# Kernel tuning notes

Hardware: AMD Instinct MI355X
Metric: run time of the kernel (lower is better)

## Reference

```python
import math
import jax, jax.numpy as jnp
import numpy as np

NUM_HEADS, RAD_PTS, LVL_PTS = 8, 4, 1
P = RAD_PTS * LVL_PTS


def setup_inputs() -> dict:
    B, Nq, Din = 2, 21760, 256
    hw = np.array([[128, 128], [64, 64], [32, 32], [16, 16]], np.int64)
    sizes = hw[:, 0] * hw[:, 1]
    offs = np.concatenate([[0], np.cumsum(sizes)[:-1]]).astype(np.int64)
    Ns = int(sizes.sum())
    map_ids = np.tile(np.repeat(np.arange(4), sizes)[None], (B, 1)).astype(np.int64)

    key = jax.random.key(0)
    ks = jax.random.split(key, 8)
    in_feats = jax.random.normal(ks[0], (B, Nq, Din), jnp.float32)
    sample_feats = jax.random.normal(ks[1], (B, Ns, Din), jnp.float32)
    sample_priors = jax.random.uniform(ks[2], (B, Nq, 2), jnp.float32)

    # sample_offsets bias: radial grid init as in the torch module
    thetas = np.arange(NUM_HEADS) * (2.0 * math.pi / NUM_HEADS)
    grid = np.stack([np.cos(thetas), np.sin(thetas), np.zeros(NUM_HEADS)], 1)
    grid = grid / np.abs(grid).max(1, keepdims=True)
    grid = np.tile(grid.reshape(NUM_HEADS, 1, 1, 3), (1, RAD_PTS, LVL_PTS, 1))
    grid = grid * np.arange(1, RAD_PTS + 1).reshape(1, RAD_PTS, 1, 1)
    bo = jnp.asarray(grid.reshape(-1), jnp.float32)

    Wo = jax.random.normal(ks[3], (NUM_HEADS * P * 3, Din), jnp.float32) * 0.01
    Wa = jax.random.normal(ks[4], (NUM_HEADS * P, Din), jnp.float32) * 0.01
    ba = jnp.zeros((NUM_HEADS * P,), jnp.float32)
    s = 1.0 / np.sqrt(Din)
    Wv = jax.random.normal(ks[5], (Din, Din), jnp.float32) * s
    bv = jnp.zeros((Din,), jnp.float32)
    Wout = jax.random.normal(ks[6], (Din, Din), jnp.float32) * s
    bout = jnp.zeros((Din,), jnp.float32)

    return dict(in_feats=in_feats, sample_priors=sample_priors, sample_feats=sample_feats,
                map_hw=jnp.asarray(hw), map_offs=jnp.asarray(offs), map_ids=jnp.asarray(map_ids),
                Wo=Wo, bo=bo, Wa=Wa, ba=ba, Wv=Wv, bv=bv, Wout=Wout, bout=bout)


def _trilinear_sample(val, map_hw, map_offs, xy, z, L):
    # val [B,Ns,H,D]; xy [B,Q,H,P,2] normalized; z [B,Q,H,P] in ~[0,1]
    B, Ns, H, D = val.shape
    Q = xy.shape[1]
    val_t = val.transpose(0, 2, 1, 3)  # [B,H,Ns,D]
    x, y = xy[..., 0], xy[..., 1]
    lvl_f = z * (L - 1)
    l0 = jnp.floor(lvl_f).astype(jnp.int32)
    wz = lvl_f - l0.astype(lvl_f.dtype)

    def gather(idx):  # idx [B,Q,H,P] int32 -> [B,Q,H,P,D]
        it = idx.transpose(0, 2, 1, 3).reshape(B, H, Q * P, 1)
        g = jnp.take_along_axis(val_t, it, axis=2)  # [B,H,Q*P,D]
        return g.reshape(B, H, Q, P, D).transpose(0, 2, 1, 3, 4)

    def sample_level(lvl):  # bilinear sample within pyramid level `lvl` (zero padding)
        valid_l = (lvl >= 0) & (lvl < L)
        lc = jnp.clip(lvl, 0, L - 1)
        Hl = map_hw[lc, 0].astype(jnp.int32)
        Wl = map_hw[lc, 1].astype(jnp.int32)
        off = map_offs[lc].astype(jnp.int32)
        xf = x * Wl.astype(x.dtype) - 0.5
        yf = y * Hl.astype(x.dtype) - 0.5
        x0 = jnp.floor(xf).astype(jnp.int32)
        y0 = jnp.floor(yf).astype(jnp.int32)
        dx = xf - x0.astype(x.dtype)
        dy = yf - y0.astype(x.dtype)
        out = jnp.zeros((B, Q, H, P, D), x.dtype)
        corners = [(x0, y0, (1 - dx) * (1 - dy)), (x0 + 1, y0, dx * (1 - dy)),
                   (x0, y0 + 1, (1 - dx) * dy), (x0 + 1, y0 + 1, dx * dy)]
        for xi, yi, w in corners:
            ok = valid_l & (xi >= 0) & (xi < Wl) & (yi >= 0) & (yi < Hl)
            idx = off + jnp.clip(yi, 0, Hl - 1) * Wl + jnp.clip(xi, 0, Wl - 1)
            out = out + gather(idx) * (w * ok.astype(x.dtype))[..., None]
        return out

    return sample_level(l0) * (1 - wz)[..., None] + sample_level(l0 + 1) * wz[..., None]


def reference(in_feats, sample_priors, sample_feats, map_hw, map_offs, map_ids,
              Wo, bo, Wa, ba, Wv, bv, Wout, bout):
    B, Nq, _ = in_feats.shape
    Ns = sample_feats.shape[1]
    L = map_hw.shape[0]
    D = Wv.shape[0] // NUM_HEADS

    val = (sample_feats @ Wv.T + bv).reshape(B, Ns, NUM_HEADS, D)
    offs = (in_feats @ Wo.T + bo).reshape(B, Nq, NUM_HEADS, P, 3)

    # sample_priors last dim == 2: normalize offsets by (W, H) of the query's map
    norm = map_hw[:, ::-1][map_ids].astype(offs.dtype)  # [B,Nq,2] (w,h)
    sample_xy = sample_priors[:, :, None, None, :2] + offs[..., :2] / norm[:, :, None, None, :]

    lvl_off = jnp.arange(LVL_PTS, dtype=offs.dtype) - 0.5 * (LVL_PTS - 1)
    z_grid = map_ids[:, :, None, None, None].astype(offs.dtype) + lvl_off  # [B,Nq,1,1,Lp]
    z_grid = jnp.broadcast_to(z_grid, (B, Nq, NUM_HEADS, RAD_PTS, LVL_PTS)).reshape(B, Nq, NUM_HEADS, P)
    sample_z = (z_grid + jnp.tanh(offs[..., 2])) / (L - 1)

    attn = jax.nn.softmax((in_feats @ Wa.T + ba).reshape(B, Nq, NUM_HEADS, P), axis=3)

    sampled = _trilinear_sample(val, map_hw, map_offs, sample_xy, sample_z, L)  # [B,Nq,H,P,D]
    attn_feats = jnp.einsum('bqhpd,bqhp->bqhd', sampled, attn).reshape(B, Nq, NUM_HEADS * D)
    return attn_feats @ Wout.T + bout
```

## Files before the change

kernel.cpp:

```cpp
#include <hip/hip_runtime.h>
#include <hip/hip_bf16.h>
#include <math.h>

typedef __bf16 bf16x8 __attribute__((ext_vector_type(8)));
typedef float f32x4 __attribute__((ext_vector_type(4)));
typedef float f32x2 __attribute__((ext_vector_type(2)));
typedef unsigned short ushort8 __attribute__((ext_vector_type(8)));

static __device__ __forceinline__ unsigned short f2bf(float f) {
    union { float f; unsigned u; } c; c.f = f;
    unsigned r = c.u + 0x7FFFu + ((c.u >> 16) & 1u);
    return (unsigned short)(r >> 16);
}

static __device__ __forceinline__ void gload_lds16(
    const unsigned short* g, unsigned short* l)
{
    __builtin_amdgcn_global_load_lds(
        (const __attribute__((address_space(1))) void*)g,
        (__attribute__((address_space(3))) void*)l, 16, 0, 0);
}

__global__ __launch_bounds__(256) void convert_weights_hist(
    const float* __restrict__ Wv, const float* __restrict__ Wo,
    const float* __restrict__ Wa, const float* __restrict__ Wout,
    const float* __restrict__ bo, const float* __restrict__ ba,
    unsigned short* __restrict__ Wv_b, unsigned short* __restrict__ Woa_b,
    unsigned short* __restrict__ Wout_b, float* __restrict__ boa,
    const float* __restrict__ priors, int* __restrict__ counts,
    int BQ, int Nq)
{
    __shared__ int cnt[16];
    if (threadIdx.x < 16) cnt[threadIdx.x] = 0;
    __syncthreads();

    int gid = blockIdx.x * blockDim.x + threadIdx.x;
    int stride = gridDim.x * blockDim.x;
    for (int i = gid; i < 163840; i += stride) {
        if (i < 65536)       Wv_b[i] = f2bf(Wv[i]);
        else if (i < 90112)  Woa_b[i - 65536] = f2bf(Wo[i - 65536]);
        else if (i < 98304)  Woa_b[i - 65536] = f2bf(Wa[i - 90112]);
        else                 Wout_b[i - 98304] = f2bf(Wout[i - 98304]);
    }
    if (gid < 96)       boa[gid] = bo[gid];
    else if (gid < 128) boa[gid] = ba[gid - 96];

    for (int q = gid; q < BQ; q += stride) {
        int b = (q >= Nq) ? 1 : 0;
        float py = priors[(size_t)q * 2 + 1];
        int band = min(7, max(0, (int)(py * 8.0f)));
        atomicAdd(&cnt[b * 8 + band], 1);
    }
    __syncthreads();
    if (threadIdx.x < 16 && cnt[threadIdx.x] > 0)
        atomicAdd(&counts[threadIdx.x], cnt[threadIdx.x]);
}

__global__ __launch_bounds__(256) void bucket_scatter(
    const float* __restrict__ priors, const int* __restrict__ counts,
    int* __restrict__ cursors, int* __restrict__ qidx, int BQ, int Nq)
{
    __shared__ int lcnt[16];
    __shared__ int lbase[16];
    const int tid = threadIdx.x;
    if (tid < 16) lcnt[tid] = 0;
    __syncthreads();
    int q = blockIdx.x * 256 + tid;
    int mybucket = 0, myslot = 0;
    bool valid = q < BQ;
    if (valid) {
        int b = (q >= Nq) ? 1 : 0;
        float py = priors[(size_t)q * 2 + 1];
        int band = min(7, max(0, (int)(py * 8.0f)));
        mybucket = b * 8 + band;
        myslot = atomicAdd(&lcnt[mybucket], 1);
    }
    __syncthreads();
    if (tid < 16) {
        int base = 0;
        #pragma unroll
        for (int i = 0; i < 16; ++i) base += (i < tid) ? counts[i] : 0;
        lbase[tid] = base + atomicAdd(&cursors[tid], lcnt[tid]);
    }
    __syncthreads();
    if (valid) qidx[lbase[mybucket] + myslot] = q;
}

template<int WM, int WN, bool A_BF16, int OUT_MODE>
__global__ __launch_bounds__(WM * WN * 64) void gemm_mfma(
    const void* __restrict__ Av, const unsigned short* __restrict__ W,
    const float* __restrict__ bias, void* __restrict__ Cv,
    int M, int N, int K, int NsPB)
{
    constexpr int BM = WM * 64;
    constexpr int BN = WN * 64;
    constexpr int BK = 64;
    constexpr int NWAVE = WM * WN;
    constexpr int NTHR = NWAVE * 64;
    constexpr int LDP = 72;
    constexpr int ASZ = A_BF16 ? (BM * 64) : (BM * LDP);

    __shared__ __align__(16) unsigned short As[ASZ];
    __shared__ __align__(16) unsigned short Bs[BN * 64];

    const int bm  = blockIdx.x * BM;
    const int bn  = blockIdx.y * BN;
    const int tid = threadIdx.x;
    const int wid = tid >> 6;
    const int wrow = wid / WN;
    const int wcol = wid % WN;
    const int lane = tid & 63;
    const int lr = lane & 15;
    const int lg = lane >> 4;
    const int lrow = lane >> 3;
    const int lc16 = (lane & 7) ^ (lrow & 7);

    f32x4 acc[4][4];
    #pragma unroll
    for (int mi = 0; mi < 4; ++mi)
        #pragma unroll
        for (int ni = 0; ni < 4; ++ni)
            acc[mi][ni] = (f32x4){0.f, 0.f, 0.f, 0.f};

    for (int kt = 0; kt < K; kt += BK) {
        #pragma unroll
        for (int c = wid; c < BN / 8; c += NWAVE) {
            const unsigned short* g =
                W + (size_t)(bn + c * 8 + lrow) * K + kt + lc16 * 8;
            gload_lds16(g, Bs + c * 512);
        }
        if (A_BF16) {
            const unsigned short* A = (const unsigned short*)Av;
            #pragma unroll
            for (int c = wid; c < BM / 8; c += NWAVE) {
                const unsigned short* g =
                    A + (size_t)(bm + c * 8 + lrow) * K + kt + lc16 * 8;
                gload_lds16(g, As + c * 512);
            }
        } else {
            const float* A = (const float*)Av;
            #pragma unroll
            for (int u = tid; u < BM * 8; u += NTHR) {
                int r = u >> 3, kb = u & 7;
                const float* src = A + (size_t)(bm + r) * K + kt + kb * 8;
                float4 f0 = *(const float4*)(src);
                float4 f1 = *(const float4*)(src + 4);
                ushort8 v;
                v[0] = f2bf(f0.x); v[1] = f2bf(f0.y);
                v[2] = f2bf(f0.z); v[3] = f2bf(f0.w);
                v[4] = f2bf(f1.x); v[5] = f2bf(f1.y);
                v[6] = f2bf(f1.z); v[7] = f2bf(f1.w);
                *(ushort8*)(As + r * LDP + kb * 8) = v;
            }
        }
        __syncthreads();

        #pragma unroll
        for (int kk = 0; kk < 2; ++kk) {
            bf16x8 fa[4], fb[4];
            #pragma unroll
            for (int mi = 0; mi < 4; ++mi) {
                int row = wrow * 64 + mi * 16 + lr;
                if (A_BF16) {
                    fa[mi] = *(const bf16x8*)(As + row * 64 +
                                              ((kk * 4 + lg) ^ (lr & 7)) * 8);
                } else {
                    fa[mi] = *(const bf16x8*)(As + row * LDP +
                                              kk * 32 + lg * 8);
                }
            }
            #pragma unroll
            for (int ni = 0; ni < 4; ++ni) {
                int row = wcol * 64 + ni * 16 + lr;
                fb[ni] = *(const bf16x8*)(Bs + row * 64 +
                                          ((kk * 4 + lg) ^ (lr & 7)) * 8);
            }
            #pragma unroll
            for (int mi = 0; mi < 4; ++mi)
                #pragma unroll
                for (int ni = 0; ni < 4; ++ni)
                    acc[mi][ni] = __builtin_amdgcn_mfma_f32_16x16x32_bf16(
                        fa[mi], fb[ni], acc[mi][ni], 0, 0, 0);
        }
        __syncthreads();
    }

    if (OUT_MODE == 2) {
        const int b = bm / NsPB;
        const int ns_base = bm - b * NsPB;
        #pragma unroll
        for (int ni = 0; ni < 4; ++ni) {
            int col = wcol * 64 + ni * 16 + lr;
            int h   = col >> 5;
            int ch  = col & 31;
            float bv = bias[col];
            unsigned short* dst = (unsigned short*)Cv +
                (size_t)(b * 8 + h) * NsPB * 32 + ch;
            #pragma unroll
            for (int mi = 0; mi < 4; ++mi) {
                #pragma unroll
                for (int r = 0; r < 4; ++r) {
                    int ns = ns_base + mi * 16 + lg * 4 + r;
                    dst[(size_t)ns * 32] = f2bf(acc[mi][ni][r] + bv);
                }
            }
        }
    } else {
        #pragma unroll
        for (int ni = 0; ni < 4; ++ni) {
            int col = bn + wcol * 64 + ni * 16 + lr;
            float bv = bias[col];
            #pragma unroll
            for (int mi = 0; mi < 4; ++mi) {
                #pragma unroll
                for (int r = 0; r < 4; ++r) {
                    int row = bm + wrow * 64 + mi * 16 + lg * 4 + r;
                    if (OUT_MODE == 1) {
                        ((unsigned short*)Cv)[(size_t)row * N + col] =
                            f2bf(acc[mi][ni][r] + bv);
                    } else {
                        ((float*)Cv)[(size_t)row * N + col] = acc[mi][ni][r] + bv;
                    }
                }
            }
        }
    }
}

__global__ __launch_bounds__(256) void msda_sample_kernel(
    const float* __restrict__ C1,
    const float* __restrict__ priors,
    const unsigned short* __restrict__ val,
    const int*   __restrict__ map_hw,
    const int*   __restrict__ map_offs,
    const int*   __restrict__ map_ids,
    const int*   __restrict__ qidx,
    unsigned short* __restrict__ out,
    int Nq, int Ns)
{
    const int swz  = (blockIdx.x & 7) * (gridDim.x >> 3) + (blockIdx.x >> 3);
    const int wvi  = threadIdx.x >> 6;
    const int lane = threadIdx.x & 63;
    const int qbase = swz * 16 + wvi * 4;

    __shared__ __align__(16) float s_rec[4][4][4][128];

    const int hp = lane >> 1;
    const int sl = lane & 1;

    int bq4[4];
    #pragma unroll
    for (int qq = 0; qq < 4; ++qq) bq4[qq] = qidx[qbase + qq];

    float o0[4], o1[4], o2[4], lgt[4], px[4], py[4];
    int bb[4], lid[4];
    #pragma unroll
    for (int qq = 0; qq < 4; ++qq) {
        const int bq = bq4[qq];
        const int b  = (bq >= Nq) ? 1 : 0;
        const int q  = bq - b * Nq;
        bb[qq] = b;
        const float* sc = C1 + (size_t)bq * 128;
        o0[qq]  = sc[hp * 3 + 0];
        o1[qq]  = sc[hp * 3 + 1];
        o2[qq]  = sc[hp * 3 + 2];
        lgt[qq] = sc[96 + hp];
        px[qq]  = priors[(size_t)bq * 2 + 0];
        py[qq]  = priors[(size_t)bq * 2 + 1];
        lid[qq] = map_ids[(size_t)b * Ns + q];
    }

    #pragma unroll
    for (int qq = 0; qq < 4; ++qq) {
        float logit = lgt[qq];
        float m = logit;
        m = fmaxf(m, __shfl_xor(m, 2));
        m = fmaxf(m, __shfl_xor(m, 4));
        float e = expf(logit - m);
        float s = e;
        s += __shfl_xor(s, 2);
        s += __shfl_xor(s, 4);
        float attnw = e / s;

        int Hq = map_hw[lid[qq] * 2 + 0];
        int Wq = map_hw[lid[qq] * 2 + 1];
        float x = px[qq] + o0[qq] / (float)Wq;
        float y = py[qq] + o1[qq] / (float)Hq;

        float lvl_f = (float)lid[qq] + tanhf(o2[qq]);
        float l0f = floorf(lvl_f);
        int   l0  = (int)l0f;
        float wz  = lvl_f - l0f;

        const int   lv = l0 + sl;
        const float wl = sl ? wz : (1.0f - wz);
        float w4[4];
        int   i4[4];
        if (lv >= 0 && lv < 4) {
            int Hs  = map_hw[lv * 2 + 0];
            int Ws  = map_hw[lv * 2 + 1];
            int off = map_offs[lv];
            float xf = x * (float)Ws - 0.5f;
            float yf = y * (float)Hs - 0.5f;
            float x0f = floorf(xf), y0f = floorf(yf);
            int   x0  = (int)x0f,  y0  = (int)y0f;
            float dx = xf - x0f, dy = yf - y0f;
            #pragma unroll
            for (int j = 0; j < 4; ++j) {
                int xi = x0 + (j & 1);
                int yi = y0 + (j >> 1);
                float w = ((j & 1) ? dx : 1.0f - dx) *
                          ((j >> 1) ? dy : 1.0f - dy);
                bool ok = (xi >= 0) && (xi < Ws) && (yi >= 0) && (yi < Hs);
                w4[j] = ok ? (w * wl * attnw) : 0.0f;
                i4[j] = ok ? ((off + yi * Ws + xi) << 6) : 0;
            }
        } else {
            #pragma unroll
            for (int j = 0; j < 4; ++j) { w4[j] = 0.0f; i4[j] = 0; }
        }
        f32x4 wrec = {w4[0], w4[1], w4[2], w4[3]};
        f32x4 irec = {__int_as_float(i4[0]), __int_as_float(i4[1]),
                      __int_as_float(i4[2]), __int_as_float(i4[3])};
        *(f32x4*)&s_rec[wvi][qq][sl][hp * 4]     = wrec;
        *(f32x4*)&s_rec[wvi][qq][2 + sl][hp * 4] = irec;
    }
    asm volatile("s_waitcnt lgkmcnt(0)" ::: "memory");

    const int p2 = lane & 1;
    const int d8 = (lane >> 1) & 3;
    const int h  = lane >> 3;

    #pragma unroll
    for (int qq = 0; qq < 4; ++qq) {
        const char* vbase =
            (const char*)(val + (size_t)(bb[qq] * 8 + h) * Ns * 32) + d8 * 16;

        f32x2 acc2[4];
        #pragma unroll
        for (int k = 0; k < 4; ++k) acc2[k] = (f32x2){0.f, 0.f};

        #pragma unroll
        for (int pp = 0; pp < 2; ++pp) {
            const int hpg = h * 4 + p2 + pp * 2;
            f32x4 wlo = *(const f32x4*)&s_rec[wvi][qq][0][hpg * 4];
            f32x4 whi = *(const f32x4*)&s_rec[wvi][qq][1][hpg * 4];
            f32x4 xlo = *(const f32x4*)&s_rec[wvi][qq][2][hpg * 4];
            f32x4 xhi = *(const f32x4*)&s_rec[wvi][qq][3][hpg * 4];

            uint4 u[8];
            #pragma unroll
            for (int j = 0; j < 4; ++j)
                u[j] = *(const uint4*)(vbase + __float_as_int(xlo[j]));
            #pragma unroll
            for (int j = 0; j < 4; ++j)
                u[4 + j] = *(const uint4*)(vbase + __float_as_int(xhi[j]));

            #pragma unroll
            for (int j = 0; j < 8; ++j) {
                float w = (j < 4) ? wlo[j] : whi[j - 4];
                f32x2 w2 = {w, w};
                unsigned ua[4] = {u[j].x, u[j].y, u[j].z, u[j].w};
                #pragma unroll
                for (int k = 0; k < 4; ++k) {
                    union { unsigned uu; float f; } lo, hi;
                    lo.uu = ua[k] << 16;
                    hi.uu = ua[k] & 0xffff0000u;
                    f32x2 v2 = {lo.f, hi.f};
                    acc2[k] += w2 * v2;
                }
            }
        }

        #pragma unroll
        for (int k = 0; k < 4; ++k) {
            acc2[k][0] += __shfl_xor(acc2[k][0], 1);
            acc2[k][1] += __shfl_xor(acc2[k][1], 1);
        }

        if (p2 == 0) {
            ushort8 o;
            #pragma unroll
            for (int k = 0; k < 4; ++k) {
                o[2 * k]     = f2bf(acc2[k][0]);
                o[2 * k + 1] = f2bf(acc2[k][1]);
            }
            *(ushort8*)(out + (size_t)bq4[qq] * 256 + h * 32 + d8 * 8) = o;
        }
    }
}

extern "C" void kernel_launch(void* const* d_in, const int* in_sizes, int n_in,
                              void* d_out, int out_size, void* d_ws, size_t ws_size,
                              hipStream_t stream) {
    const float* in_feats      = (const float*)d_in[0];
    const float* sample_priors = (const float*)d_in[1];
    const float* sample_feats  = (const float*)d_in[2];
    const int*   map_hw        = (const int*)d_in[3];
    const int*   map_offs      = (const int*)d_in[4];
    const int*   map_ids       = (const int*)d_in[5];
    const float* Wo            = (const float*)d_in[6];
    const float* bo            = (const float*)d_in[7];
    const float* Wa            = (const float*)d_in[8];
    const float* ba            = (const float*)d_in[9];
    const float* Wv            = (const float*)d_in[10];
    const float* bv            = (const float*)d_in[11];
    const float* Wout          = (const float*)d_in[12];
    const float* bout          = (const float*)d_in[13];
    float* out = (float*)d_out;

    const int B = 2, Nq = 21760, Din = 256;
    const int Ns = in_sizes[2] / (B * Din);
    const int BQ = B * Nq;

    unsigned short* val = (unsigned short*)d_out;
    float* C1 = (float*)d_ws;
    unsigned short* af = (unsigned short*)((char*)d_ws + (size_t)BQ * 128 * 4);
    char* wbase = (char*)d_ws + (size_t)BQ * 128 * 4 + (size_t)BQ * 256 * 2;
    unsigned short* Wv_b   = (unsigned short*)wbase;
    unsigned short* Woa_b  = Wv_b + 65536;
    unsigned short* Wout_b = Woa_b + 32768;
    float* boa = (float*)(Wout_b + 65536);
    int* bws  = (int*)(boa + 128);
    int* qidx = bws + 32;

    hipMemsetAsync(bws, 0, 128, stream);

    convert_weights_hist<<<dim3(160), dim3(256), 0, stream>>>(
        Wv, Wo, Wa, Wout, bo, ba, Wv_b, Woa_b, Wout_b, boa,
        sample_priors, bws, BQ, Nq);

    bucket_scatter<<<dim3((BQ + 255) / 256), dim3(256), 0, stream>>>(
        sample_priors, bws, bws + 16, qidx, BQ, Nq);

    gemm_mfma<1, 4, false, 2><<<dim3(BQ / 64, 1), dim3(256), 0, stream>>>(
        sample_feats, Wv_b, bv, val, B * Ns, 256, Din, Ns);

    gemm_mfma<1, 2, false, 0><<<dim3(BQ / 64, 1), dim3(128), 0, stream>>>(
        in_feats, Woa_b, boa, C1, BQ, 128, Din, Ns);

    msda_sample_kernel<<<dim3(BQ / 16), dim3(256), 0, stream>>>(
        C1, sample_priors, val, map_hw, map_offs, map_ids, qidx, af, Nq, Ns);

    gemm_mfma<1, 4, true, 0><<<dim3(BQ / 64, 1), dim3(256), 0, stream>>>(
        af, Wout_b, bout, out, BQ, 256, Din, Ns);
}
```

Baseline: 115.9 us.

## Process one query per wave in sampling kernel with coalesced C1 loads

The sampling kernel now assigns one query per wavefront instead of four, launching four times as many blocks. Each wave loads the query's 128-float C1 row coalesced and redistributes it with ds_bpermute. Scalar per-query values are broadcast via readfirstlane. Precise expf, division and tanhf are replaced with fast exp/rcp approximations. This aims to raise memory-level parallelism and cut redundant scalar loads, at the cost of more blocks and slightly lower numeric precision.

```diff
diff --git a/kernel.cpp b/kernel.cpp
--- a/kernel.cpp
+++ b/kernel.cpp
@@ -241,53 +241,71 @@
     const int swz  = (blockIdx.x & 7) * (gridDim.x >> 3) + (blockIdx.x >> 3);
     const int wvi  = threadIdx.x >> 6;
     const int lane = threadIdx.x & 63;
-    const int qbase = swz * 16 + wvi * 4;
-
-    __shared__ __align__(16) float s_rec[4][4][4][128];
+
+    __shared__ __align__(16) float s_rec[4][4][128];
+
+    int bq_l = 0;
+    if (lane == 0) bq_l = qidx[swz * 4 + wvi];
+    const int bq = __builtin_amdgcn_readfirstlane(bq_l);
+    const int b  = (bq >= Nq) ? 1 : 0;
+    const int q  = bq - b * Nq;
+
+    const float* sc = C1 + (size_t)bq * 128;
+    const float cA = sc[lane];
+    const float cB = sc[64 + lane];
+
+    float pxv = 0.f, pyv = 0.f;
+    int lid_l = 0;
+    if (lane == 0) {
+        float2 pr = *(const float2*)(priors + (size_t)bq * 2);
+        pxv = pr.x; pyv = pr.y;
+        lid_l = map_ids[(size_t)b * Ns + q];
+    }
+    const float px = __uint_as_float(
+        __builtin_amdgcn_readfirstlane(__float_as_uint(pxv)));
+    const float py = __uint_as_float(
+        __builtin_amdgcn_readfirstlane(__float_as_uint(pyv)));
+    const int lid = __builtin_amdgcn_readfirstlane(lid_l);
 
     const int hp = lane >> 1;
     const int sl = lane & 1;
 
-    int bq4[4];
-    #pragma unroll
-    for (int qq = 0; qq < 4; ++qq) bq4[qq] = qidx[qbase + qq];
-
-    float o0[4], o1[4], o2[4], lgt[4], px[4], py[4];
-    int bb[4], lid[4];
-    #pragma unroll
-    for (int qq = 0; qq < 4; ++qq) {
-        const int bq = bq4[qq];
-        const int b  = (bq >= Nq) ? 1 : 0;
-        const int q  = bq - b * Nq;
-        bb[qq] = b;
-        const float* sc = C1 + (size_t)bq * 128;
-        o0[qq]  = sc[hp * 3 + 0];
-        o1[qq]  = sc[hp * 3 + 1];
-        o2[qq]  = sc[hp * 3 + 2];
-        lgt[qq] = sc[96 + hp];
-        px[qq]  = priors[(size_t)bq * 2 + 0];
-        py[qq]  = priors[(size_t)bq * 2 + 1];
-        lid[qq] = map_ids[(size_t)b * Ns + q];
-    }
-
-    #pragma unroll
-    for (int qq = 0; qq < 4; ++qq) {
-        float logit = lgt[qq];
-        float m = logit;
-        m = fmaxf(m, __shfl_xor(m, 2));
+    const int iA = __float_as_int(cA);
+    const int iB = __float_as_int(cB);
+    float o0, o1, o2;
+    {
+        int i0 = hp * 3 + 0, i1 = hp * 3 + 1, i2 = hp * 3 + 2;
+        int a0 = __builtin_amdgcn_ds_bpermute(i0 << 2, iA);
+        int b0 = __builtin_amdgcn_ds_bpermute((i0 - 64) << 2, iB);
+        int a1 = __builtin_amdgcn_ds_bpermute(i1 << 2, iA);
+        int b1 = __builtin_amdgcn_ds_bpermute((i1 - 64) << 2, iB);
+        int a2 = __builtin_amdgcn_ds_bpermute(i2 << 2, iA);
+        int b2 = __builtin_amdgcn_ds_bpermute((i2 - 64) << 2, iB);
+        o0 = __int_as_float(i0 < 64 ? a0 : b0);
+        o1 = __int_as_float(i1 < 64 ? a1 : b1);
+        o2 = __int_as_float(i2 < 64 ? a2 : b2);
+    }
+    const float logit = __int_as_float(
+        __builtin_amdgcn_ds_bpermute((32 + hp) << 2, iB));
+
+    {
+        float m = fmaxf(logit, __shfl_xor(logit, 2));
         m = fmaxf(m, __shfl_xor(m, 4));
-        float e = expf(logit - m);
+        float e = __expf(logit - m);
         float s = e;
         s += __shfl_xor(s, 2);
         s += __shfl_xor(s, 4);
-        float attnw = e / s;
-
-        int Hq = map_hw[lid[qq] * 2 + 0];
-        int Wq = map_hw[lid[qq] * 2 + 1];
-        float x = px[qq] + o0[qq] / (float)Wq;
-        float y = py[qq] + o1[qq] / (float)Hq;
-
-        float lvl_f = (float)lid[qq] + tanhf(o2[qq]);
+        float attnw = e * __builtin_amdgcn_rcpf(s);
+
+        int Hq = map_hw[lid * 2 + 0];
+        int Wq = map_hw[lid * 2 + 1];
+        float x = px + o0 * __builtin_amdgcn_rcpf((float)Wq);
+        float y = py + o1 * __builtin_amdgcn_rcpf((float)Hq);
+
+        float ex = __expf(2.0f * o2);
+        float th = 1.0f - 2.0f * __builtin_amdgcn_rcpf(ex + 1.0f);
+
+        float lvl_f = (float)lid + th;
         float l0f = floorf(lvl_f);
         int   l0  = (int)l0f;
         float wz  = lvl_f - l0f;
@@ -322,71 +340,67 @@
         f32x4 wrec = {w4[0], w4[1], w4[2], w4[3]};
         f32x4 irec = {__int_as_float(i4[0]), __int_as_float(i4[1]),
                       __int_as_float(i4[2]), __int_as_float(i4[3])};
-        *(f32x4*)&s_rec[wvi][qq][sl][hp * 4]     = wrec;
-        *(f32x4*)&s_rec[wvi][qq][2 + sl][hp * 4] = irec;
+        *(f32x4*)&s_rec[wvi][sl][hp * 4]     = wrec;
+        *(f32x4*)&s_rec[wvi][2 + sl][hp * 4] = irec;
     }
     asm volatile("s_waitcnt lgkmcnt(0)" ::: "memory");
 
     const int p2 = lane & 1;
     const int d8 = (lane >> 1) & 3;
     const int h  = lane >> 3;
-
+    const char* vbase = (const char*)(val + (size_t)(b * 8 + h) * Ns * 32)
+                        + d8 * 16;
+
+    f32x2 acc2[4];
     #pragma unroll
-    for (int qq = 0; qq < 4; ++qq) {
-        const char* vbase =
-            (const char*)(val + (size_t)(bb[qq] * 8 + h) * Ns * 32) + d8 * 16;
-
-        f32x2 acc2[4];
-        #pragma unroll
-        for (int k = 0; k < 4; ++k) acc2[k] = (f32x2){0.f, 0.f};
-
-        #pragma unroll
-        for (int pp = 0; pp < 2; ++pp) {
-            const int hpg = h * 4 + p2 + pp * 2;
-            f32x4 wlo = *(const f32x4*)&s_rec[wvi][qq][0][hpg * 4];
-            f32x4 whi = *(const f32x4*)&s_rec[wvi][qq][1][hpg * 4];
-            f32x4 xlo = *(const f32x4*)&s_rec[wvi][qq][2][hpg * 4];
-            f32x4 xhi = *(const f32x4*)&s_rec[wvi][qq][3][hpg * 4];
-
-            uint4 u[8];
-            #pragma unroll
-            for (int j = 0; j < 4; ++j)
-                u[j] = *(const uint4*)(vbase + __float_as_int(xlo[j]));
-            #pragma unroll
-            for (int j = 0; j < 4; ++j)
-                u[4 + j] = *(const uint4*)(vbase + __float_as_int(xhi[j]));
-
-            #pragma unroll
-            for (int j = 0; j < 8; ++j) {
-                float w = (j < 4) ? wlo[j] : whi[j - 4];
-                f32x2 w2 = {w, w};
-                unsigned ua[4] = {u[j].x, u[j].y, u[j].z, u[j].w};
-                #pragma unroll
-                for (int k = 0; k < 4; ++k) {
-                    union { unsigned uu; float f; } lo, hi;
-                    lo.uu = ua[k] << 16;
-                    hi.uu = ua[k] & 0xffff0000u;
-                    f32x2 v2 = {lo.f, hi.f};
-                    acc2[k] += w2 * v2;
-                }
-            }
-        }
-
+    for (int k = 0; k < 4; ++k) acc2[k] = (f32x2){0.f, 0.f};
+
+    #pragma unroll
+    for (int pp = 0; pp < 2; ++pp) {
+        const int hpg = h * 4 + p2 + pp * 2;
+        f32x4 wlo = *(const f32x4*)&s_rec[wvi][0][hpg * 4];
+        f32x4 whi = *(const f32x4*)&s_rec[wvi][1][hpg * 4];
+        f32x4 xlo = *(const f32x4*)&s_rec[wvi][2][hpg * 4];
+        f32x4 xhi = *(const f32x4*)&s_rec[wvi][3][hpg * 4];
+
+        uint4 u[8];
+        #pragma unroll
+        for (int j = 0; j < 4; ++j)
+            u[j] = *(const uint4*)(vbase + __float_as_int(xlo[j]));
+        #pragma unroll
+        for (int j = 0; j < 4; ++j)
+            u[4 + j] = *(const uint4*)(vbase + __float_as_int(xhi[j]));
+
+        #pragma unroll
+        for (int j = 0; j < 8; ++j) {
+            float w = (j < 4) ? wlo[j] : whi[j - 4];
+            f32x2 w2 = {w, w};
+            unsigned ua[4] = {u[j].x, u[j].y, u[j].z, u[j].w};
+            #pragma unroll
+            for (int k = 0; k < 4; ++k) {
+                union { unsigned uu; float f; } lo, hi;
+                lo.uu = ua[k] << 16;
+                hi.uu = ua[k] & 0xffff0000u;
+                f32x2 v2 = {lo.f, hi.f};
+                acc2[k] += w2 * v2;
+            }
+        }
+    }
+
+    #pragma unroll
+    for (int k = 0; k < 4; ++k) {
+        acc2[k][0] += __shfl_xor(acc2[k][0], 1);
+        acc2[k][1] += __shfl_xor(acc2[k][1], 1);
+    }
+
+    if (p2 == 0) {
+        ushort8 o;
         #pragma unroll
         for (int k = 0; k < 4; ++k) {
-            acc2[k][0] += __shfl_xor(acc2[k][0], 1);
-            acc2[k][1] += __shfl_xor(acc2[k][1], 1);
-        }
-
-        if (p2 == 0) {
-            ushort8 o;
-            #pragma unroll
-            for (int k = 0; k < 4; ++k) {
-                o[2 * k]     = f2bf(acc2[k][0]);
-                o[2 * k + 1] = f2bf(acc2[k][1]);
-            }
-            *(ushort8*)(out + (size_t)bq4[qq] * 256 + h * 32 + d8 * 8) = o;
-        }
+            o[2 * k]     = f2bf(acc2[k][0]);
+            o[2 * k + 1] = f2bf(acc2[k][1]);
+        }
+        *(ushort8*)(out + (size_t)bq * 256 + h * 32 + d8 * 8) = o;
     }
 }
 
@@ -439,7 +453,7 @@
     gemm_mfma<1, 2, false, 0><<<dim3(BQ / 64, 1), dim3(128), 0, stream>>>(
         in_feats, Woa_b, boa, C1, BQ, 128, Din, Ns);
 
-    msda_sample_kernel<<<dim3(BQ / 16), dim3(256), 0, stream>>>(
+    msda_sample_kernel<<<dim3(BQ / 4), dim3(256), 0, stream>>>(
         C1, sample_priors, val, map_hw, map_offs, map_ids, qidx, af, Nq, Ns);
 
     gemm_mfma<1, 4, true, 0><<<dim3(BQ / 64, 1), dim3(256), 0, stream>>>(
```

Result: faster. 110.2 us (-4.9%).
